# Performance work log

Hardware: AMD Instinct MI355X
Metric: run time of the kernel (lower is better)

Reference implementation:

```python
import jax, jax.numpy as jnp
import numpy as np

N_TX, N_USER, N_MERCH = 100000, 20000, 5000
E = 400000
F_IN, H, L = 32, 256, 2


def setup_inputs() -> dict:
    key = jax.random.key(0)
    ks = jax.random.split(key, 24)
    p = lambda k, s: 0.02 * jax.random.normal(k, s, dtype=jnp.float32)
    return {
        "x_tx": jax.random.normal(ks[0], (N_TX, F_IN), dtype=jnp.float32),
        "x_user": jax.random.normal(ks[1], (N_USER, H), dtype=jnp.float32),
        "x_merch": jax.random.normal(ks[2], (N_MERCH, H), dtype=jnp.float32),
        # input projection
        "Wp": p(ks[3], (F_IN, H)), "bp": jnp.zeros((H,), jnp.float32),
        # per-layer, per-edge-type SAGEConv params: lin_l (neighbor, with bias) and lin_r (root, no bias)
        "Wl": p(ks[4], (L, 4, H, H)), "bl": jnp.zeros((L, 4, H), jnp.float32),
        "Wr": p(ks[5], (L, 4, H, H)),
        # classifier head
        "Wc1": p(ks[6], (H, H // 2)), "bc1": jnp.zeros((H // 2,), jnp.float32),
        "Wc2": p(ks[7], (H // 2, 1)), "bc2": jnp.zeros((1,), jnp.float32),
        # revenue head
        "Wv1": p(ks[8], (H, H // 2)), "bv1": jnp.zeros((H // 2,), jnp.float32),
        "Wv2": p(ks[9], (H // 2, 1)), "bv2": jnp.zeros((1,), jnp.float32),
        # edge lists (src, dst) per relation
        "e_ut_src": jax.random.randint(ks[10], (E,), 0, N_USER, dtype=jnp.int32),
        "e_ut_dst": jax.random.randint(ks[11], (E,), 0, N_TX, dtype=jnp.int32),
        "e_tm_src": jax.random.randint(ks[12], (E,), 0, N_TX, dtype=jnp.int32),
        "e_tm_dst": jax.random.randint(ks[13], (E,), 0, N_MERCH, dtype=jnp.int32),
        "e_mt_src": jax.random.randint(ks[14], (E,), 0, N_MERCH, dtype=jnp.int32),
        "e_mt_dst": jax.random.randint(ks[15], (E,), 0, N_TX, dtype=jnp.int32),
        "e_tu_src": jax.random.randint(ks[16], (E,), 0, N_TX, dtype=jnp.int32),
        "e_tu_dst": jax.random.randint(ks[17], (E,), 0, N_USER, dtype=jnp.int32),
    }


def _seg_mean(x_src, src, dst, n_dst):
    # gather source features per edge, scatter-mean into destinations
    msg = x_src[src]                                        # [E, H]
    s = jax.ops.segment_sum(msg, dst, num_segments=n_dst)   # [n_dst, H]
    cnt = jax.ops.segment_sum(jnp.ones((dst.shape[0],), x_src.dtype), dst, num_segments=n_dst)
    return s / jnp.maximum(cnt, 1.0)[:, None]


def _sage(x_src, x_dst, src, dst, Wl, bl, Wr):
    # PyG SAGEConv: lin_l(mean_neighbors) + lin_r(x_dst)
    m = _seg_mean(x_src, src, dst, x_dst.shape[0])
    return m @ Wl + bl + x_dst @ Wr


def reference(x_tx, x_user, x_merch, Wp, bp, Wl, bl, Wr,
              Wc1, bc1, Wc2, bc2, Wv1, bv1, Wv2, bv2,
              e_ut_src, e_ut_dst, e_tm_src, e_tm_dst,
              e_mt_src, e_mt_dst, e_tu_src, e_tu_dst):
    xt = x_tx @ Wp + bp          # input_proj on 'transaction'
    xu, xm = x_user, x_merch     # already hidden_dim -> used as-is
    for l in range(L):
        t_from_u = _sage(xu, xt, e_ut_src, e_ut_dst, Wl[l, 0], bl[l, 0], Wr[l, 0])
        m_from_t = _sage(xt, xm, e_tm_src, e_tm_dst, Wl[l, 1], bl[l, 1], Wr[l, 1])
        t_from_m = _sage(xm, xt, e_mt_src, e_mt_dst, Wl[l, 2], bl[l, 2], Wr[l, 2])
        u_from_t = _sage(xt, xu, e_tu_src, e_tu_dst, Wl[l, 3], bl[l, 3], Wr[l, 3])
        # HeteroConv aggr='mean' over edge types per destination, then ReLU (dropout = identity in eval)
        xt = jax.nn.relu(0.5 * (t_from_u + t_from_m))
        xm = jax.nn.relu(m_from_t)
        xu = jax.nn.relu(u_from_t)
    fraud_logits = (jax.nn.relu(xt @ Wc1 + bc1) @ Wc2 + bc2)[:, 0]
    revenue_pred = (jax.nn.relu(xt @ Wv1 + bv1) @ Wv2 + bv2)[:, 0]
    return fraud_logits, revenue_pred
```

## Files before the change

### kernel.cpp

```cpp
#include <hip/hip_runtime.h>

#define NTX 100000
#define NUSER 20000
#define NMERCH 5000
#define HD 256
#define ROWPAD 128

using u16 = unsigned short;
typedef __attribute__((ext_vector_type(8))) short bf16x8;
typedef __attribute__((ext_vector_type(4))) float f32x4;

__device__ __forceinline__ u16 f2bf(float f){
  unsigned u = __float_as_uint(f);
  unsigned r = (u + 0x7FFFu + ((u >> 16) & 1u)) >> 16;
  return (u16)r;
}
__device__ __forceinline__ float bf2f(u16 b){
  return __uint_as_float(((unsigned)b) << 16);
}
__device__ __forceinline__ unsigned pk2(float a, float b){
  return (unsigned)f2bf(a) | ((unsigned)f2bf(b) << 16);
}

__device__ __forceinline__ void gather4(const u16* __restrict__ T, const int* __restrict__ ss,
    int j0, int j1, int lane, int c, float& o0, float& o1, float& o2, float& o3){
  float a0=0,a1=0,a2=0,a3=0, b0=0,b1=0,b2=0,b3=0;
  float c0=0,c1=0,c2=0,c3=0, d0=0,d1=0,d2=0,d3=0;
  for (int base = j0; base < j1; base += 64){
    int n = j1 - base; if (n > 64) n = 64;
    int idx = ss[base + (lane < n ? lane : 0)];
    for (int jj = 0; jj < n; jj += 4){
      int s0 = __shfl(idx, jj);
      int s1 = __shfl(idx, jj+1);
      int s2 = __shfl(idx, jj+2);
      int s3 = __shfl(idx, jj+3);
      ushort4 v0 = *(const ushort4*)(T + (size_t)s0*HD + c);
      ushort4 v1 = *(const ushort4*)(T + (size_t)s1*HD + c);
      ushort4 v2 = *(const ushort4*)(T + (size_t)s2*HD + c);
      ushort4 v3 = *(const ushort4*)(T + (size_t)s3*HD + c);
      a0 += bf2f(v0.x); a1 += bf2f(v0.y); a2 += bf2f(v0.z); a3 += bf2f(v0.w);
      if (jj+1 < n){ b0 += bf2f(v1.x); b1 += bf2f(v1.y); b2 += bf2f(v1.z); b3 += bf2f(v1.w); }
      if (jj+2 < n){ c0 += bf2f(v2.x); c1 += bf2f(v2.y); c2 += bf2f(v2.z); c3 += bf2f(v2.w); }
      if (jj+3 < n){ d0 += bf2f(v3.x); d1 += bf2f(v3.y); d2 += bf2f(v3.z); d3 += bf2f(v3.w); }
    }
  }
  o0 += (a0+b0)+(c0+d0); o1 += (a1+b1)+(c1+d1);
  o2 += (a2+b2)+(c2+d2); o3 += (a3+b3)+(c3+d3);
}

__device__ __forceinline__ int rel_n(int y){ return y==0?NTX: y==1?NMERCH: y==2?NTX:NUSER; }
__device__ __forceinline__ int rel_coff(int y){ return y==0?0: y==1?100000: y==2?105000:205000; }
__device__ __forceinline__ int rel_rpoff(int y){ return y==0?0: y==1?100001: y==2?105002:205003; }
__device__ __forceinline__ int rel_shift(int y){ return y==0?11: y==1?8: y==2?11:10; }
__device__ __forceinline__ int rel_np(int y){ return y==0?49: y==1?20: y==2?49:20; }
#define ECH 128
#define PSTW 72

__global__ __launch_bounds__(256) void csrA_kernel(const int* __restrict__ d0p, const int* __restrict__ d1p,
    const int* __restrict__ d2p, const int* __restrict__ d3p, int nE, int* __restrict__ PC){
  int y = blockIdx.y;
  const int* dst = y==0?d0p: y==1?d1p: y==2?d2p:d3p;
  int shift = rel_shift(y);
  __shared__ int cc[64];
  int t = threadIdx.x;
  if (t < 64) cc[t] = 0;
  __syncthreads();
  int CH = (nE + ECH - 1)/ECH;
  int e0 = blockIdx.x*CH, e1 = e0 + CH; if (e1 > nE) e1 = nE;
  for (int e = e0 + t*4; e < e1; e += 1024){
    int a = dst[e];
    int b = (e+1 < e1) ? dst[e+1] : -1;
    int c = (e+2 < e1) ? dst[e+2] : -1;
    int d = (e+3 < e1) ? dst[e+3] : -1;
    atomicAdd(&cc[a>>shift], 1);
    if (b >= 0) atomicAdd(&cc[b>>shift], 1);
    if (c >= 0) atomicAdd(&cc[c>>shift], 1);
    if (d >= 0) atomicAdd(&cc[d>>shift], 1);
  }
  __syncthreads();
  if (t < 64) PC[(((size_t)y*ECH + blockIdx.x)<<6) + t] = cc[t];
}

__global__ void csrB_kernel(int* __restrict__ PC, int* __restrict__ PST, int* __restrict__ RP, int nE){
  int y = blockIdx.y;
  int np = rel_np(y);
  int t = threadIdx.x;
  __shared__ int sh[64];
  int run = 0;
  if (t < np){
    for (int c = 0; c < ECH; ++c){
      size_t idx = (((size_t)y*ECH + c)<<6) + t;
      int v = PC[idx]; PC[idx] = run; run += v;
    }
  }
  sh[t] = run;
  __syncthreads();
  if (t == 0){
    int acc = 0;
    for (int i = 0; i < np; ++i){ int v = sh[i]; sh[i] = acc; acc += v; }
    PST[y*PSTW + np] = nE;
    RP[rel_rpoff(y) + rel_n(y)] = nE;
  }
  __syncthreads();
  if (t < np){
    int base = sh[t];
    PST[y*PSTW + t] = base;
    for (int c = 0; c < ECH; ++c){
      size_t idx = (((size_t)y*ECH + c)<<6) + t;
      PC[idx] += base;
    }
  }
}

__global__ __launch_bounds__(256) void csrC_kernel(
    const int* __restrict__ s0p, const int* __restrict__ d0p,
    const int* __restrict__ s1p, const int* __restrict__ d1p,
    const int* __restrict__ s2p, const int* __restrict__ d2p,
    const int* __restrict__ s3p, const int* __restrict__ d3p,
    const int* __restrict__ PC, int* __restrict__ EB, int nE){
  int y = blockIdx.y;
  const int* src = y==0?s0p: y==1?s1p: y==2?s2p:s3p;
  const int* dst = y==0?d0p: y==1?d1p: y==2?d2p:d3p;
  int shift = rel_shift(y);
  int mask = (1<<shift) - 1;
  __shared__ int cur[64];
  int t = threadIdx.x;
  if (t < 64) cur[t] = PC[(((size_t)y*ECH + blockIdx.x)<<6) + t];
  __syncthreads();
  int CH = (nE + ECH - 1)/ECH;
  int e0 = blockIdx.x*CH, e1 = e0 + CH; if (e1 > nE) e1 = nE;
  int* eb = EB + (size_t)y*nE;
  for (int e = e0 + t*4; e < e1; e += 1024){
    #pragma unroll
    for (int u = 0; u < 4; ++u){
      int ee = e + u;
      if (ee < e1){
        int d = dst[ee], s = src[ee];
        int pos = atomicAdd(&cur[d>>shift], 1);
        eb[pos] = ((d & mask) << 17) | s;
      }
    }
  }
}

__global__ __launch_bounds__(256) void csrD_kernel(const int* __restrict__ EB, const int* __restrict__ PST,
    int* __restrict__ RP, float* __restrict__ INV,
    int* __restrict__ ss0, int* __restrict__ ss1, int* __restrict__ ss2, int* __restrict__ ss3, int nE){
  int y = blockIdx.y;
  int np = rel_np(y);
  int part = blockIdx.x;
  if (part >= np) return;
  int shift = rel_shift(y);
  int n = rel_n(y);
  int gbase = part << shift;
  int len = n - gbase; int range = 1 << shift; if (len > range) len = range;
  __shared__ int cnt[2048];
  __shared__ int curs[2048];
  __shared__ int sh[256];
  int t = threadIdx.x;
  for (int i = t; i < len; i += 256) cnt[i] = 0;
  __syncthreads();
  const int* eb = EB + (size_t)y*nE;
  int j0 = PST[y*PSTW + part], j1 = PST[y*PSTW + part + 1];
  for (int j = j0 + t*4; j < j1; j += 1024){
    int a = eb[j];
    int b = (j+1 < j1) ? eb[j+1] : -1;
    int c = (j+2 < j1) ? eb[j+2] : -1;
    int d = (j+3 < j1) ? eb[j+3] : -1;
    atomicAdd(&cnt[a>>17], 1);
    if (b >= 0) atomicAdd(&cnt[b>>17], 1);
    if (c >= 0) atomicAdd(&cnt[c>>17], 1);
    if (d >= 0) atomicAdd(&cnt[d>>17], 1);
  }
  __syncthreads();
  int base8 = t*8;
  int vals[8]; int tsum = 0;
  #pragma unroll
  for (int u = 0; u < 8; ++u){
    int i = base8 + u;
    int v = (i < len) ? cnt[i] : 0;
    vals[u] = tsum; tsum += v;
  }
  sh[t] = tsum;
  __syncthreads();
  for (int o = 1; o < 256; o <<= 1){
    int v = (t >= o) ? sh[t-o] : 0;
    __syncthreads();
    sh[t] += v;
    __syncthreads();
  }
  int tbase = j0 + sh[t] - tsum;
  int rpo = rel_rpoff(y) + gbase;
  int ivo = rel_coff(y) + gbase;
  #pragma unroll
  for (int u = 0; u < 8; ++u){
    int i = base8 + u;
    if (i < len){
      int start = tbase + vals[u];
      curs[i] = start;
      RP[rpo + i] = start;
      INV[ivo + i] = 1.f/fmaxf((float)cnt[i], 1.f);
    }
  }
  __syncthreads();
  int* ss = y==0?ss0: y==1?ss1: y==2?ss2:ss3;
  for (int j = j0 + t*4; j < j1; j += 1024){
    #pragma unroll
    for (int u = 0; u < 4; ++u){
      int jj = j + u;
      if (jj < j1){
        int pk = eb[jj];
        int pos = atomicAdd(&curs[pk>>17], 1);
        ss[pos] = pk & 0x1FFFF;
      }
    }
  }
}

__global__ __launch_bounds__(256) void wprep_kernel(const float* __restrict__ Wl, const float* __restrict__ Wr,
    const float* __restrict__ Wp, const float* __restrict__ Wc1, const float* __restrict__ Wv1,
    const float* __restrict__ bc1, const float* __restrict__ bv1,
    u16* __restrict__ WTl, u16* __restrict__ WTr1, u16* __restrict__ WTr3, u16* __restrict__ WT02,
    u16* __restrict__ WTH, u16* __restrict__ WTp, float* __restrict__ bH){
  int y = blockIdx.y;
  int i = blockIdx.x*256 + threadIdx.x;
  if (y < 8){
    if (i < 65536){ int k=i>>8, n=i&255; WTl[(size_t)y*65536 + n*256 + k] = f2bf(Wl[(size_t)y*65536 + i]); }
  } else if (y < 10){
    int l = y-8;
    if (i < 65536){ int k=i>>8, n=i&255; WTr1[(size_t)l*65536 + n*256 + k] = f2bf(Wr[(size_t)(l*4+1)*65536 + i]); }
  } else if (y < 12){
    int l = y-10;
    if (i < 65536){ int k=i>>8, n=i&255; WTr3[(size_t)l*65536 + n*256 + k] = f2bf(Wr[(size_t)(l*4+3)*65536 + i]); }
  } else if (y < 14){
    int l = y-12;
    if (i < 65536){ int k=i>>8, n=i&255;
      WT02[(size_t)l*65536 + n*256 + k] = f2bf(Wr[(size_t)(l*4+0)*65536 + i] + Wr[(size_t)(l*4+2)*65536 + i]); }
  } else if (y == 14){
    if (i < 65536){ int k=i>>8, n=i&255;
      float v = (n < 128) ? Wc1[k*128 + n] : Wv1[k*128 + (n-128)];
      WTH[(size_t)n*256 + k] = f2bf(v); }
  } else {
    if (i < 8192){ int k=i>>8, n=i&255; WTp[(size_t)n*32 + k] = f2bf(Wp[i]); }
    if (i < 256) bH[i] = (i < 128) ? bc1[i] : bv1[i-128];
  }
}

__global__ __launch_bounds__(256) void cvt2_kernel(const float* __restrict__ xu,
    const float* __restrict__ xm, u16* __restrict__ XU, u16* __restrict__ XM){
  int y = blockIdx.y;
  const float* in = y==0?xu:xm;
  u16* out = y==0?XU:XM;
  int n4 = y==0?NUSER*HD/4:NMERCH*HD/4;
  int i = blockIdx.x*256 + threadIdx.x;
  if (i >= n4) return;
  float4 v = ((const float4*)in)[i];
  ushort4 o; o.x = f2bf(v.x); o.y = f2bf(v.y); o.z = f2bf(v.z); o.w = f2bf(v.w);
  ((ushort4*)out)[i] = o;
}

#define STAGE_STORE(EXPR_BF16)                                                     \
  {                                                                                \
    int rsub = (lane >> 4) << 2;                                                   \
    int wh = w >> 1;                                                               \
    for (int h = 0; h < 2; ++h){                                                   \
      if (wh == h){                                                                \
        _Pragma("unroll")                                                          \
        for (int j = 0; j < 4; ++j){                                               \
          int cl = wn + j*16 + lm;                                                 \
          _Pragma("unroll")                                                        \
          for (int i = 0; i < 4; ++i){                                             \
            int lr = i*16 + rsub;                                                  \
            _Pragma("unroll")                                                      \
            for (int r = 0; r < 4; ++r) smem[(lr+r)*136 + cl] = (EXPR_BF16);       \
          }                                                                        \
        }                                                                          \
      }                                                                            \
      __syncthreads();                                                             \
      int lr2 = threadIdx.x >> 2;                                                  \
      int cb = (threadIdx.x & 3) << 5;                                             \
      int grow = m0 + h*64 + lr2;                                                  \
      if (grow < M){                                                               \
        _Pragma("unroll")                                                          \
        for (int kq = 0; kq < 4; ++kq)                                             \
          *(uint4*)(C + (size_t)grow*256 + n0 + cb + kq*8) =                       \
              *(const uint4*)&smem[lr2*136 + cb + kq*8];                           \
      }                                                                            \
      __syncthreads();                                                             \
    }                                                                              \
  }

__global__ __launch_bounds__(256) void proj_gemm_kernel(const float* __restrict__ A, const u16* __restrict__ WT,
    const float* __restrict__ bias, u16* __restrict__ C, int M){
  __shared__ u16 smem[10240];
  u16* As = smem; u16* Bs = smem + 5120;
  int m0 = blockIdx.x * 128, n0 = blockIdx.y * 128;
  int t = threadIdx.x;
  int w = t >> 6, lane = t & 63;
  int wm = (w >> 1) << 6, wn = (w & 1) << 6;
  int lm = lane & 15;
  int lk = (lane >> 4) << 3;
  int sr = t >> 1, sc = (t & 1) << 4;
  float4 f0 = {0,0,0,0}, f1 = {0,0,0,0}, f2 = {0,0,0,0}, f3 = {0,0,0,0};
  if (m0 + sr < M){
    const float* ap = A + (size_t)(m0+sr)*32 + sc;
    f0 = *(const float4*)(ap+0); f1 = *(const float4*)(ap+4);
    f2 = *(const float4*)(ap+8); f3 = *(const float4*)(ap+12);
  }
  uint4 q0, q1;
  q0.x = pk2(f0.x,f0.y); q0.y = pk2(f0.z,f0.w); q0.z = pk2(f1.x,f1.y); q0.w = pk2(f1.z,f1.w);
  q1.x = pk2(f2.x,f2.y); q1.y = pk2(f2.z,f2.w); q1.z = pk2(f3.x,f3.y); q1.w = pk2(f3.z,f3.w);
  *(uint4*)&As[sr*40 + sc] = q0;
  *(uint4*)&As[sr*40 + sc+8] = q1;
  const u16* bp_ = WT + (size_t)(n0+sr)*32 + sc;
  *(uint4*)&Bs[sr*40 + sc]   = *(const uint4*)(bp_);
  *(uint4*)&Bs[sr*40 + sc+8] = *(const uint4*)(bp_ + 8);
  __syncthreads();
  bf16x8 af[4], bf[4];
  #pragma unroll
  for (int i = 0; i < 4; ++i) af[i] = *(const bf16x8*)&As[(wm + i*16 + lm)*40 + lk];
  #pragma unroll
  for (int j = 0; j < 4; ++j) bf[j] = *(const bf16x8*)&Bs[(wn + j*16 + lm)*40 + lk];
  f32x4 acc[4][4] = {};
  #pragma unroll
  for (int i = 0; i < 4; ++i)
    #pragma unroll
    for (int j = 0; j < 4; ++j)
      acc[i][j] = __builtin_amdgcn_mfma_f32_16x16x32_bf16(af[i], bf[j], acc[i][j], 0, 0, 0);
  __syncthreads();
  float bcol[4];
  #pragma unroll
  for (int j = 0; j < 4; ++j) bcol[j] = bias[n0 + wn + j*16 + lm];
  STAGE_STORE(f2bf(acc[i][j][r] + bcol[j]))
}

__global__ __launch_bounds__(256) void gemm_nb_kernel(const u16* __restrict__ A, const u16* __restrict__ WT,
    u16* __restrict__ C, int M){
  __shared__ u16 smem[10240];
  u16* As = smem; u16* Bs = smem + 5120;
  int m0 = blockIdx.x * 128, n0 = blockIdx.y * 128;
  if (m0 >= M) return;
  int t = threadIdx.x;
  int w = t >> 6, lane = t & 63;
  int wm = (w >> 1) << 6, wn = (w & 1) << 6;
  int lm = lane & 15;
  int lk = (lane >> 4) << 3;
  f32x4 acc[4][4] = {};
  int sr0 = t >> 2, sk0 = (t & 3) << 3;
  int sr1 = sr0 + 64;
  for (int k0 = 0; k0 < 256; k0 += 32){
    uint4 a0 = *(const uint4*)(A  + (size_t)(m0+sr0)*256 + k0 + sk0);
    uint4 a1 = *(const uint4*)(A  + (size_t)(m0+sr1)*256 + k0 + sk0);
    uint4 b0 = *(const uint4*)(WT + (size_t)(n0+sr0)*256 + k0 + sk0);
    uint4 b1 = *(const uint4*)(WT + (size_t)(n0+sr1)*256 + k0 + sk0);
    *(uint4*)&As[sr0*40 + sk0] = a0;
    *(uint4*)&As[sr1*40 + sk0] = a1;
    *(uint4*)&Bs[sr0*40 + sk0] = b0;
    *(uint4*)&Bs[sr1*40 + sk0] = b1;
    __syncthreads();
    bf16x8 af[4], bf[4];
    #pragma unroll
    for (int i = 0; i < 4; ++i) af[i] = *(const bf16x8*)&As[(wm + i*16 + lm)*40 + lk];
    #pragma unroll
    for (int j = 0; j < 4; ++j) bf[j] = *(const bf16x8*)&Bs[(wn + j*16 + lm)*40 + lk];
    #pragma unroll
    for (int i = 0; i < 4; ++i)
      #pragma unroll
      for (int j = 0; j < 4; ++j)
        acc[i][j] = __builtin_amdgcn_mfma_f32_16x16x32_bf16(af[i], bf[j], acc[i][j], 0, 0, 0);
    __syncthreads();
  }
  STAGE_STORE(f2bf(acc[i][j][r]))
}

__global__ __launch_bounds__(256) void pair_gemm_kernel(
    const u16* __restrict__ A0, const u16* __restrict__ W0, u16* __restrict__ C0, int M0,
    const u16* __restrict__ A1, const u16* __restrict__ W1, u16* __restrict__ C1, int M1){
  int z = blockIdx.z;
  const u16* A = z ? A1 : A0;
  const u16* WT = z ? W1 : W0;
  u16* C = z ? C1 : C0;
  int M = z ? M1 : M0;
  int m0 = blockIdx.x * 128, n0 = blockIdx.y * 128;
  if (m0 >= M) return;
  __shared__ u16 smem[10240];
  u16* As = smem; u16* Bs = smem + 5120;
  int t = threadIdx.x;
  int w = t >> 6, lane = t & 63;
  int wm = (w >> 1) << 6, wn = (w & 1) << 6;
  int lm = lane & 15;
  int lk = (lane >> 4) << 3;
  f32x4 acc[4][4] = {};
  int sr0 = t >> 2, sk0 = (t & 3) << 3;
  int sr1 = sr0 + 64;
  for (int k0 = 0; k0 < 256; k0 += 32){
    uint4 a0 = *(const uint4*)(A  + (size_t)(m0+sr0)*256 + k0 + sk0);
    uint4 a1 = *(const uint4*)(A  + (size_t)(m0+sr1)*256 + k0 + sk0);
    uint4 b0 = *(const uint4*)(WT + (size_t)(n0+sr0)*256 + k0 + sk0);
    uint4 b1 = *(const uint4*)(WT + (size_t)(n0+sr1)*256 + k0 + sk0);
    *(uint4*)&As[sr0*40 + sk0] = a0;
    *(uint4*)&As[sr1*40 + sk0] = a1;
    *(uint4*)&Bs[sr0*40 + sk0] = b0;
    *(uint4*)&Bs[sr1*40 + sk0] = b1;
    __syncthreads();
    bf16x8 af[4], bf[4];
    #pragma unroll
    for (int i = 0; i < 4; ++i) af[i] = *(const bf16x8*)&As[(wm + i*16 + lm)*40 + lk];
    #pragma unroll
    for (int j = 0; j < 4; ++j) bf[j] = *(const bf16x8*)&Bs[(wn + j*16 + lm)*40 + lk];
    #pragma unroll
    for (int i = 0; i < 4; ++i)
      #pragma unroll
      for (int j = 0; j < 4; ++j)
        acc[i][j] = __builtin_amdgcn_mfma_f32_16x16x32_bf16(af[i], bf[j], acc[i][j], 0, 0, 0);
    __syncthreads();
  }
  STAGE_STORE(f2bf(acc[i][j][r]))
}

__global__ __launch_bounds__(256) void pair_gemm2_kernel(
    const u16* __restrict__ G0, const u16* __restrict__ X0, const u16* __restrict__ Wa0, const u16* __restrict__ Wb0,
    const float* __restrict__ b0, u16* __restrict__ C0, int M0,
    const u16* __restrict__ G1, const u16* __restrict__ X1, const u16* __restrict__ Wa1, const u16* __restrict__ Wb1,
    const float* __restrict__ b1, u16* __restrict__ C1, int M1){
  int z = blockIdx.z;
  const u16* G  = z ? G1 : G0;
  const u16* X  = z ? X1 : X0;
  const u16* Wa = z ? Wa1 : Wa0;
  const u16* Wb = z ? Wb1 : Wb0;
  const float* bias = z ? b1 : b0;
  u16* C = z ? C1 : C0;
  int M = z ? M1 : M0;
  int m0 = blockIdx.x * 128, n0 = blockIdx.y * 128;
  if (m0 >= M) return;
  __shared__ u16 smem[10240];
  u16* As = smem; u16* Bs = smem + 5120;
  int t = threadIdx.x;
  int w = t >> 6, lane = t & 63;
  int wm = (w >> 1) << 6, wn = (w & 1) << 6;
  int lm = lane & 15;
  int lk = (lane >> 4) << 3;
  f32x4 acc[4][4] = {};
  int sr0 = t >> 2, sk0 = (t & 3) << 3;
  int sr1 = sr0 + 64;
  for (int k0 = 0; k0 < 512; k0 += 32){
    const u16* A  = (k0 < 256) ? G : X;
    const u16* WT = (k0 < 256) ? Wa : Wb;
    int kk = k0 & 255;
    uint4 a0 = *(const uint4*)(A  + (size_t)(m0+sr0)*256 + kk + sk0);
    uint4 a1 = *(const uint4*)(A  + (size_t)(m0+sr1)*256 + kk + sk0);
    uint4 b0_ = *(const uint4*)(WT + (size_t)(n0+sr0)*256 + kk + sk0);
    uint4 b1_ = *(const uint4*)(WT + (size_t)(n0+sr1)*256 + kk + sk0);
    *(uint4*)&As[sr0*40 + sk0] = a0;
    *(uint4*)&As[sr1*40 + sk0] = a1;
    *(uint4*)&Bs[sr0*40 + sk0] = b0_;
    *(uint4*)&Bs[sr1*40 + sk0] = b1_;
    __syncthreads();
    bf16x8 af[4], bf[4];
    #pragma unroll
    for (int i = 0; i < 4; ++i) af[i] = *(const bf16x8*)&As[(wm + i*16 + lm)*40 + lk];
    #pragma unroll
    for (int j = 0; j < 4; ++j) bf[j] = *(const bf16x8*)&Bs[(wn + j*16 + lm)*40 + lk];
    #pragma unroll
    for (int i = 0; i < 4; ++i)
      #pragma unroll
      for (int j = 0; j < 4; ++j)
        acc[i][j] = __builtin_amdgcn_mfma_f32_16x16x32_bf16(af[i], bf[j], acc[i][j], 0, 0, 0);
    __syncthreads();
  }
  float bcol[4];
  #pragma unroll
  for (int j = 0; j < 4; ++j) bcol[j] = bias[n0 + wn + j*16 + lm];
  STAGE_STORE(f2bf(fmaxf(acc[i][j][r] + bcol[j], 0.f)))
}

__global__ __launch_bounds__(256) void gather_pair_kernel(const u16* __restrict__ XT,
    const int* __restrict__ rp0, const int* __restrict__ ss0, const float* __restrict__ inv0,
    u16* __restrict__ out0, int M0,
    const int* __restrict__ rp1, const int* __restrict__ ss1, const float* __restrict__ inv1,
    u16* __restrict__ out1, int M1){
  int y = blockIdx.y;
  const int* rp = y ? rp1 : rp0;
  const int* ss = y ? ss1 : ss0;
  const float* inv = y ? inv1 : inv0;
  u16* out = y ? out1 : out0;
  int M = y ? M1 : M0;
  int d = blockIdx.x*4 + (threadIdx.x >> 6);
  if (d >= M) return;
  int lane = threadIdx.x & 63;
  int c = lane << 2;
  float o0=0,o1=0,o2=0,o3=0;
  gather4(XT, ss, rp[d], rp[d+1], lane, c, o0, o1, o2, o3);
  float sc = inv[d];
  ushort4 o; o.x = f2bf(o0*sc); o.y = f2bf(o1*sc); o.z = f2bf(o2*sc); o.w = f2bf(o3*sc);
  *(ushort4*)(out + (size_t)d*HD + c) = o;
}

__global__ __launch_bounds__(256) void fused_tx_kernel(const u16* __restrict__ ACCb,
    const u16* __restrict__ Tu, const u16* __restrict__ Tm,
    const int* __restrict__ rpu, const int* __restrict__ ssu, const float* __restrict__ invu,
    const int* __restrict__ rpm, const int* __restrict__ ssm, const float* __restrict__ invm,
    const float* __restrict__ b0, const float* __restrict__ b2, u16* __restrict__ XT, int M){
  int d = blockIdx.x*4 + (threadIdx.x >> 6);
  if (d >= M) return;
  int lane = threadIdx.x & 63;
  int c = lane << 2;
  ushort4 av = *(const ushort4*)(ACCb + (size_t)d*HD + c);
  float r0 = bf2f(av.x), r1 = bf2f(av.y), r2 = bf2f(av.z), r3 = bf2f(av.w);
  {
    float s0=0,s1=0,s2=0,s3=0;
    gather4(Tu, ssu, rpu[d], rpu[d+1], lane, c, s0, s1, s2, s3);
    float sc = invu[d];
    r0 += s0*sc; r1 += s1*sc; r2 += s2*sc; r3 += s3*sc;
  }
  {
    float s0=0,s1=0,s2=0,s3=0;
    gather4(Tm, ssm, rpm[d], rpm[d+1], lane, c, s0, s1, s2, s3);
    float sc = invm[d];
    r0 += s0*sc; r1 += s1*sc; r2 += s2*sc; r3 += s3*sc;
  }
  float4 bb0 = *(const float4*)(b0 + c);
  float4 bb2 = *(const float4*)(b2 + c);
  ushort4 o;
  o.x = f2bf(fmaxf(0.5f*(r0 + bb0.x + bb2.x), 0.f));
  o.y = f2bf(fmaxf(0.5f*(r1 + bb0.y + bb2.y), 0.f));
  o.z = f2bf(fmaxf(0.5f*(r2 + bb0.z + bb2.z), 0.f));
  o.w = f2bf(fmaxf(0.5f*(r3 + bb0.w + bb2.w), 0.f));
  *(ushort4*)(XT + (size_t)d*HD + c) = o;
}

__global__ __launch_bounds__(256) void fused_head_kernel(const u16* __restrict__ A, const u16* __restrict__ BT,
    const float* __restrict__ bias, const float* __restrict__ Wc2, const float* __restrict__ bc2,
    const float* __restrict__ Wv2, const float* __restrict__ bv2, float* __restrict__ out, int M){
  __shared__ u16 As[128*40];
  __shared__ u16 Bs[128*40];
  __shared__ float hpart[128];
  int m0 = blockIdx.x * 128, n0 = blockIdx.y * 128;
  int t = threadIdx.x;
  int w = t >> 6, lane = t & 63;
  int wm = (w >> 1) << 6, wn = (w & 1) << 6;
  int lm = lane & 15;
  int lk = (lane >> 4) << 3;
  if (t < 128) hpart[t] = 0.f;
  f32x4 acc[4][4] = {};
  int sr0 = t >> 2, sk0 = (t & 3) << 3;
  int sr1 = sr0 + 64;
  for (int k0 = 0; k0 < 256; k0 += 32){
    uint4 a0 = *(const uint4*)(A  + (size_t)(m0+sr0)*256 + k0 + sk0);
    uint4 a1 = *(const uint4*)(A  + (size_t)(m0+sr1)*256 + k0 + sk0);
    uint4 b0 = *(const uint4*)(BT + (size_t)(n0+sr0)*256 + k0 + sk0);
    uint4 b1 = *(const uint4*)(BT + (size_t)(n0+sr1)*256 + k0 + sk0);
    *(uint4*)&As[sr0*40 + sk0] = a0;
    *(uint4*)&As[sr1*40 + sk0] = a1;
    *(uint4*)&Bs[sr0*40 + sk0] = b0;
    *(uint4*)&Bs[sr1*40 + sk0] = b1;
    __syncthreads();
    bf16x8 af[4], bf[4];
    #pragma unroll
    for (int i = 0; i < 4; ++i) af[i] = *(const bf16x8*)&As[(wm + i*16 + lm)*40 + lk];
    #pragma unroll
    for (int j = 0; j < 4; ++j) bf[j] = *(const bf16x8*)&Bs[(wn + j*16 + lm)*40 + lk];
    #pragma unroll
    for (int i = 0; i < 4; ++i)
      #pragma unroll
      for (int j = 0; j < 4; ++j)
        acc[i][j] = __builtin_amdgcn_mfma_f32_16x16x32_bf16(af[i], bf[j], acc[i][j], 0, 0, 0);
    __syncthreads();
  }
  const float* w2 = blockIdx.y ? Wv2 : Wc2;
  float badd = blockIdx.y ? bv2[0] : bc2[0];
  size_t outoff = blockIdx.y ? (size_t)M : 0;
  int rsub = (lane >> 4) << 2;
  float w2v[4], bv[4];
  #pragma unroll
  for (int j = 0; j < 4; ++j){
    w2v[j] = w2[wn + j*16 + lm];
    bv[j]  = bias[n0 + wn + j*16 + lm];
  }
  #pragma unroll
  for (int i = 0; i < 4; ++i){
    #pragma unroll
    for (int r = 0; r < 4; ++r){
      float p = 0.f;
      #pragma unroll
      for (int j = 0; j < 4; ++j) p += fmaxf(acc[i][j][r] + bv[j], 0.f) * w2v[j];
      p += __shfl_xor(p, 1); p += __shfl_xor(p, 2);
      p += __shfl_xor(p, 4); p += __shfl_xor(p, 8);
      if (lm == 0) atomicAdd(&hpart[wm + i*16 + rsub + r], p);
    }
  }
  __syncthreads();
  if (t < 128){
    int row = m0 + t;
    if (row < M) out[outoff + row] = hpart[t] + badd;
  }
}

extern "C" void kernel_launch(void* const* d_in, const int* in_sizes, int n_in,
                              void* d_out, int out_size, void* d_ws, size_t ws_size,
                              hipStream_t stream){
  const float* x_tx   = (const float*)d_in[0];
  const float* x_user = (const float*)d_in[1];
  const float* x_merch= (const float*)d_in[2];
  const float* Wp  = (const float*)d_in[3];
  const float* bp  = (const float*)d_in[4];
  const float* Wl  = (const float*)d_in[5];
  const float* bl  = (const float*)d_in[6];
  const float* Wr  = (const float*)d_in[7];
  const float* Wc1 = (const float*)d_in[8];
  const float* bc1 = (const float*)d_in[9];
  const float* Wc2 = (const float*)d_in[10];
  const float* bc2 = (const float*)d_in[11];
  const float* Wv1 = (const float*)d_in[12];
  const float* bv1 = (const float*)d_in[13];
  const float* Wv2 = (const float*)d_in[14];
  const float* bv2 = (const float*)d_in[15];
  const int* e_ut_s = (const int*)d_in[16];
  const int* e_ut_d = (const int*)d_in[17];
  const int* e_tm_s = (const int*)d_in[18];
  const int* e_tm_d = (const int*)d_in[19];
  const int* e_mt_s = (const int*)d_in[20];
  const int* e_mt_d = (const int*)d_in[21];
  const int* e_tu_s = (const int*)d_in[22];
  const int* e_tu_d = (const int*)d_in[23];
  float* out = (float*)d_out;
  const int NE = in_sizes[16];

  char* p = (char*)d_ws;
  auto take = [&](size_t bytes)->char*{ char* r = p; p += (bytes + 255) & ~(size_t)255; return r; };
  u16*   XT    = (u16*)  take((size_t)(NTX+ROWPAD)*HD*2);
  u16*   ACCb  = (u16*)  take((size_t)(NTX+ROWPAD)*HD*2);
  u16*   Tu    = (u16*)  take((size_t)NUSER*HD*2);
  u16*   Tm    = (u16*)  take((size_t)NMERCH*HD*2);
  u16*   AGGU  = (u16*)  take((size_t)(NUSER+ROWPAD)*HD*2);
  u16*   AGGM  = (u16*)  take((size_t)(NMERCH+ROWPAD)*HD*2);
  u16*   XU0   = (u16*)  take((size_t)(NUSER+ROWPAD)*HD*2);
  u16*   XU1   = (u16*)  take((size_t)(NUSER+ROWPAD)*HD*2);
  u16*   XM0   = (u16*)  take((size_t)(NMERCH+ROWPAD)*HD*2);
  u16*   XM1   = (u16*)  take((size_t)(NMERCH+ROWPAD)*HD*2);
  float* INV   = (float*)take((size_t)225000*4);
  int*   RP    = (int*)  take((size_t)225008*4);
  int*   SS_ut = (int*)  take((size_t)NE*4);
  int*   SS_tm = (int*)  take((size_t)NE*4);
  int*   SS_mt = (int*)  take((size_t)NE*4);
  int*   SS_tu = (int*)  take((size_t)NE*4);
  int*   PC    = (int*)  take((size_t)4*ECH*64*4);
  int*   PST   = (int*)  take((size_t)4*PSTW*4);
  int*   EB    = (int*)  take((size_t)4*NE*4);
  u16*   WTp   = (u16*)  take((size_t)32*256*2);
  u16*   WTl   = (u16*)  take((size_t)8*65536*2);
  u16*   WTr1  = (u16*)  take((size_t)2*65536*2);
  u16*   WTr3  = (u16*)  take((size_t)2*65536*2);
  u16*   WT02  = (u16*)  take((size_t)2*65536*2);
  u16*   WTH   = (u16*)  take((size_t)65536*2);
  float* bH    = (float*)take((size_t)256*4);

  float* inv_ut = INV,  *inv_tm = INV+100000, *inv_mt = INV+105000, *inv_tu = INV+205000;
  int*   rp_ut  = RP,   *rp_tm  = RP+100001,  *rp_mt  = RP+105002,  *rp_tu  = RP+205003;

  csrA_kernel<<<dim3(ECH,4),256,0,stream>>>(e_ut_d, e_tm_d, e_mt_d, e_tu_d, NE, PC);
  csrB_kernel<<<dim3(1,4),64,0,stream>>>(PC, PST, RP, NE);
  csrC_kernel<<<dim3(ECH,4),256,0,stream>>>(e_ut_s, e_ut_d, e_tm_s, e_tm_d, e_mt_s, e_mt_d,
      e_tu_s, e_tu_d, PC, EB, NE);
  csrD_kernel<<<dim3(49,4),256,0,stream>>>(EB, PST, RP, INV, SS_ut, SS_tm, SS_mt, SS_tu, NE);

  wprep_kernel<<<dim3(256,16),256,0,stream>>>(Wl, Wr, Wp, Wc1, Wv1, bc1, bv1,
      WTl, WTr1, WTr3, WT02, WTH, WTp, bH);

  cvt2_kernel<<<dim3(5000,2),256,0,stream>>>(x_user, x_merch, XU0, XM0);
  proj_gemm_kernel<<<dim3(782,2),256,0,stream>>>(x_tx, WTp, bp, XT, NTX);

  u16* xu_cur = XU0; u16* xu_nxt = XU1;
  u16* xm_cur = XM0; u16* xm_nxt = XM1;

  for (int l = 0; l < 2; ++l){
    const float* bl_l = bl + (size_t)l*4*256;
    u16* WTl_l = WTl + (size_t)l*4*65536;

    gather_pair_kernel<<<dim3(5000,2),256,0,stream>>>(XT,
        rp_tm, SS_tm, inv_tm, AGGM, NMERCH,
        rp_tu, SS_tu, inv_tu, AGGU, NUSER);

    pair_gemm_kernel<<<dim3(157,2,2),256,0,stream>>>(
        xu_cur, WTl_l + 0*65536, Tu, NUSER,
        xm_cur, WTl_l + 2*65536, Tm, NMERCH);

    gemm_nb_kernel<<<dim3(782,2),256,0,stream>>>(XT, WT02 + (size_t)l*65536, ACCb, NTX);
    fused_tx_kernel<<<(NTX+3)/4,256,0,stream>>>(ACCb, Tu, Tm,
        rp_ut, SS_ut, inv_ut, rp_mt, SS_mt, inv_mt,
        bl_l + 0*256, bl_l + 2*256, XT, NTX);

    pair_gemm2_kernel<<<dim3(157,2,2),256,0,stream>>>(
        AGGU, xu_cur, WTl_l + 3*65536, WTr3 + (size_t)l*65536, bl_l + 3*256, xu_nxt, NUSER,
        AGGM, xm_cur, WTl_l + 1*65536, WTr1 + (size_t)l*65536, bl_l + 1*256, xm_nxt, NMERCH);

    { u16* tmp = xu_cur; xu_cur = xu_nxt; xu_nxt = tmp; }
    { u16* tmp = xm_cur; xm_cur = xm_nxt; xm_nxt = tmp; }
  }

  fused_head_kernel<<<dim3(782,2),256,0,stream>>>(XT, WTH, bH, Wc2, bc2, Wv2, bv2, out, NTX);
}
```

Measured before the change: 542.2 us.

## Merge per-layer GEMMs and gathers into two grouped launches with ping-pong XT

Each layer's three neighbor/root GEMMs (XT·WT02, xu·Wl0, xm·Wl2) now run in one flat-grid launch. The two gathers into merchant/user plus the fused transaction update run in a second flat-grid launch. The transaction state is double-buffered so the fused update writes in place into the ACC buffer and the gathers keep reading the old XT, which removes the ordering that forced separate launches. This cuts launches per layer from four to two and lets small workloads share the GPU with large ones, at the cost of branchy block dispatch and mixed block types inside one grid.

```diff
diff --git a/kernel.cpp b/kernel.cpp
--- a/kernel.cpp
+++ b/kernel.cpp
@@ -334,12 +334,9 @@
   STAGE_STORE(f2bf(acc[i][j][r] + bcol[j]))
 }
 
-__global__ __launch_bounds__(256) void gemm_nb_kernel(const u16* __restrict__ A, const u16* __restrict__ WT,
-    u16* __restrict__ C, int M){
-  __shared__ u16 smem[10240];
+__device__ __forceinline__ void gemm_nb_body(const u16* __restrict__ A, const u16* __restrict__ WT,
+    u16* __restrict__ C, int M, int m0, int n0, u16* smem){
   u16* As = smem; u16* Bs = smem + 5120;
-  int m0 = blockIdx.x * 128, n0 = blockIdx.y * 128;
-  if (m0 >= M) return;
   int t = threadIdx.x;
   int w = t >> 6, lane = t & 63;
   int wm = (w >> 1) << 6, wn = (w & 1) << 6;
@@ -373,49 +370,91 @@
   STAGE_STORE(f2bf(acc[i][j][r]))
 }
 
-__global__ __launch_bounds__(256) void pair_gemm_kernel(
-    const u16* __restrict__ A0, const u16* __restrict__ W0, u16* __restrict__ C0, int M0,
-    const u16* __restrict__ A1, const u16* __restrict__ W1, u16* __restrict__ C1, int M1){
-  int z = blockIdx.z;
-  const u16* A = z ? A1 : A0;
-  const u16* WT = z ? W1 : W0;
-  u16* C = z ? C1 : C0;
-  int M = z ? M1 : M0;
-  int m0 = blockIdx.x * 128, n0 = blockIdx.y * 128;
-  if (m0 >= M) return;
+__global__ __launch_bounds__(256) void gemmsA_kernel(
+    const u16* __restrict__ XT, const u16* __restrict__ WT02l, u16* __restrict__ ACCb,
+    const u16* __restrict__ xu, const u16* __restrict__ Wl0, u16* __restrict__ Tu,
+    const u16* __restrict__ xm, const u16* __restrict__ Wl2, u16* __restrict__ Tm){
   __shared__ u16 smem[10240];
-  u16* As = smem; u16* Bs = smem + 5120;
-  int t = threadIdx.x;
-  int w = t >> 6, lane = t & 63;
-  int wm = (w >> 1) << 6, wn = (w & 1) << 6;
-  int lm = lane & 15;
-  int lk = (lane >> 4) << 3;
-  f32x4 acc[4][4] = {};
-  int sr0 = t >> 2, sk0 = (t & 3) << 3;
-  int sr1 = sr0 + 64;
-  for (int k0 = 0; k0 < 256; k0 += 32){
-    uint4 a0 = *(const uint4*)(A  + (size_t)(m0+sr0)*256 + k0 + sk0);
-    uint4 a1 = *(const uint4*)(A  + (size_t)(m0+sr1)*256 + k0 + sk0);
-    uint4 b0 = *(const uint4*)(WT + (size_t)(n0+sr0)*256 + k0 + sk0);
-    uint4 b1 = *(const uint4*)(WT + (size_t)(n0+sr1)*256 + k0 + sk0);
-    *(uint4*)&As[sr0*40 + sk0] = a0;
-    *(uint4*)&As[sr1*40 + sk0] = a1;
-    *(uint4*)&Bs[sr0*40 + sk0] = b0;
-    *(uint4*)&Bs[sr1*40 + sk0] = b1;
-    __syncthreads();
-    bf16x8 af[4], bf[4];
-    #pragma unroll
-    for (int i = 0; i < 4; ++i) af[i] = *(const bf16x8*)&As[(wm + i*16 + lm)*40 + lk];
-    #pragma unroll
-    for (int j = 0; j < 4; ++j) bf[j] = *(const bf16x8*)&Bs[(wn + j*16 + lm)*40 + lk];
-    #pragma unroll
-    for (int i = 0; i < 4; ++i)
-      #pragma unroll
-      for (int j = 0; j < 4; ++j)
-        acc[i][j] = __builtin_amdgcn_mfma_f32_16x16x32_bf16(af[i], bf[j], acc[i][j], 0, 0, 0);
-    __syncthreads();
-  }
-  STAGE_STORE(f2bf(acc[i][j][r]))
+  int b = blockIdx.x;
+  if (b < 1564){
+    int ny = (b >= 782) ? 1 : 0;
+    int x = b - ny*782;
+    gemm_nb_body(XT, WT02l, ACCb, NTX, x*128, ny*128, smem);
+  } else {
+    int bb = b - 1564;
+    if (bb < 314){
+      int ny = bb / 157, x = bb - ny*157;
+      gemm_nb_body(xu, Wl0, Tu, NUSER, x*128, ny*128, smem);
+    } else {
+      bb -= 314;
+      int ny = bb / 40, x = bb - ny*40;
+      gemm_nb_body(xm, Wl2, Tm, NMERCH, x*128, ny*128, smem);
+    }
+  }
+}
+
+__device__ __forceinline__ void gather_body(const u16* __restrict__ XT,
+    const int* __restrict__ rp, const int* __restrict__ ss, const float* __restrict__ inv,
+    u16* __restrict__ out, int M, int bx){
+  int d = bx*4 + (threadIdx.x >> 6);
+  if (d >= M) return;
+  int lane = threadIdx.x & 63;
+  int c = lane << 2;
+  float o0=0,o1=0,o2=0,o3=0;
+  gather4(XT, ss, rp[d], rp[d+1], lane, c, o0, o1, o2, o3);
+  float sc = inv[d];
+  ushort4 o; o.x = f2bf(o0*sc); o.y = f2bf(o1*sc); o.z = f2bf(o2*sc); o.w = f2bf(o3*sc);
+  *(ushort4*)(out + (size_t)d*HD + c) = o;
+}
+
+__device__ __forceinline__ void fused_tx_body(const u16* __restrict__ ACCb,
+    const u16* __restrict__ Tu, const u16* __restrict__ Tm,
+    const int* __restrict__ rpu, const int* __restrict__ ssu, const float* __restrict__ invu,
+    const int* __restrict__ rpm, const int* __restrict__ ssm, const float* __restrict__ invm,
+    const float* __restrict__ b0, const float* __restrict__ b2, u16* __restrict__ XT, int M, int bx){
+  int d = bx*4 + (threadIdx.x >> 6);
+  if (d >= M) return;
+  int lane = threadIdx.x & 63;
+  int c = lane << 2;
+  ushort4 av = *(const ushort4*)(ACCb + (size_t)d*HD + c);
+  float r0 = bf2f(av.x), r1 = bf2f(av.y), r2 = bf2f(av.z), r3 = bf2f(av.w);
+  {
+    float s0=0,s1=0,s2=0,s3=0;
+    gather4(Tu, ssu, rpu[d], rpu[d+1], lane, c, s0, s1, s2, s3);
+    float sc = invu[d];
+    r0 += s0*sc; r1 += s1*sc; r2 += s2*sc; r3 += s3*sc;
+  }
+  {
+    float s0=0,s1=0,s2=0,s3=0;
+    gather4(Tm, ssm, rpm[d], rpm[d+1], lane, c, s0, s1, s2, s3);
+    float sc = invm[d];
+    r0 += s0*sc; r1 += s1*sc; r2 += s2*sc; r3 += s3*sc;
+  }
+  float4 bb0 = *(const float4*)(b0 + c);
+  float4 bb2 = *(const float4*)(b2 + c);
+  ushort4 o;
+  o.x = f2bf(fmaxf(0.5f*(r0 + bb0.x + bb2.x), 0.f));
+  o.y = f2bf(fmaxf(0.5f*(r1 + bb0.y + bb2.y), 0.f));
+  o.z = f2bf(fmaxf(0.5f*(r2 + bb0.z + bb2.z), 0.f));
+  o.w = f2bf(fmaxf(0.5f*(r3 + bb0.w + bb2.w), 0.f));
+  *(ushort4*)(XT + (size_t)d*HD + c) = o;
+}
+
+__global__ __launch_bounds__(256) void gatherB_kernel(const u16* __restrict__ XTc,
+    const int* __restrict__ rp_tm, const int* __restrict__ ss_tm, const float* __restrict__ inv_tm, u16* __restrict__ AGGM,
+    const int* __restrict__ rp_tu, const int* __restrict__ ss_tu, const float* __restrict__ inv_tu, u16* __restrict__ AGGU,
+    u16* __restrict__ ACCb, const u16* __restrict__ Tu, const u16* __restrict__ Tm,
+    const int* __restrict__ rp_ut, const int* __restrict__ ss_ut, const float* __restrict__ inv_ut,
+    const int* __restrict__ rp_mt, const int* __restrict__ ss_mt, const float* __restrict__ inv_mt,
+    const float* __restrict__ b0, const float* __restrict__ b2){
+  int b = blockIdx.x;
+  if (b < 1250){
+    gather_body(XTc, rp_tm, ss_tm, inv_tm, AGGM, NMERCH, b);
+  } else if (b < 6250){
+    gather_body(XTc, rp_tu, ss_tu, inv_tu, AGGU, NUSER, b - 1250);
+  } else {
+    fused_tx_body(ACCb, Tu, Tm, rp_ut, ss_ut, inv_ut, rp_mt, ss_mt, inv_mt, b0, b2, ACCb, NTX, b - 6250);
+  }
 }
 
 __global__ __launch_bounds__(256) void pair_gemm2_kernel(
@@ -472,61 +511,6 @@
   #pragma unroll
   for (int j = 0; j < 4; ++j) bcol[j] = bias[n0 + wn + j*16 + lm];
   STAGE_STORE(f2bf(fmaxf(acc[i][j][r] + bcol[j], 0.f)))
-}
-
-__global__ __launch_bounds__(256) void gather_pair_kernel(const u16* __restrict__ XT,
-    const int* __restrict__ rp0, const int* __restrict__ ss0, const float* __restrict__ inv0,
-    u16* __restrict__ out0, int M0,
-    const int* __restrict__ rp1, const int* __restrict__ ss1, const float* __restrict__ inv1,
-    u16* __restrict__ out1, int M1){
-  int y = blockIdx.y;
-  const int* rp = y ? rp1 : rp0;
-  const int* ss = y ? ss1 : ss0;
-  const float* inv = y ? inv1 : inv0;
-  u16* out = y ? out1 : out0;
-  int M = y ? M1 : M0;
-  int d = blockIdx.x*4 + (threadIdx.x >> 6);
-  if (d >= M) return;
-  int lane = threadIdx.x & 63;
-  int c = lane << 2;
-  float o0=0,o1=0,o2=0,o3=0;
-  gather4(XT, ss, rp[d], rp[d+1], lane, c, o0, o1, o2, o3);
-  float sc = inv[d];
-  ushort4 o; o.x = f2bf(o0*sc); o.y = f2bf(o1*sc); o.z = f2bf(o2*sc); o.w = f2bf(o3*sc);
-  *(ushort4*)(out + (size_t)d*HD + c) = o;
-}
-
-__global__ __launch_bounds__(256) void fused_tx_kernel(const u16* __restrict__ ACCb,
-    const u16* __restrict__ Tu, const u16* __restrict__ Tm,
-    const int* __restrict__ rpu, const int* __restrict__ ssu, const float* __restrict__ invu,
-    const int* __restrict__ rpm, const int* __restrict__ ssm, const float* __restrict__ invm,
-    const float* __restrict__ b0, const float* __restrict__ b2, u16* __restrict__ XT, int M){
-  int d = blockIdx.x*4 + (threadIdx.x >> 6);
-  if (d >= M) return;
-  int lane = threadIdx.x & 63;
-  int c = lane << 2;
-  ushort4 av = *(const ushort4*)(ACCb + (size_t)d*HD + c);
-  float r0 = bf2f(av.x), r1 = bf2f(av.y), r2 = bf2f(av.z), r3 = bf2f(av.w);
-  {
-    float s0=0,s1=0,s2=0,s3=0;
-    gather4(Tu, ssu, rpu[d], rpu[d+1], lane, c, s0, s1, s2, s3);
-    float sc = invu[d];
-    r0 += s0*sc; r1 += s1*sc; r2 += s2*sc; r3 += s3*sc;
-  }
-  {
-    float s0=0,s1=0,s2=0,s3=0;
-    gather4(Tm, ssm, rpm[d], rpm[d+1], lane, c, s0, s1, s2, s3);
-    float sc = invm[d];
-    r0 += s0*sc; r1 += s1*sc; r2 += s2*sc; r3 += s3*sc;
-  }
-  float4 bb0 = *(const float4*)(b0 + c);
-  float4 bb2 = *(const float4*)(b2 + c);
-  ushort4 o;
-  o.x = f2bf(fmaxf(0.5f*(r0 + bb0.x + bb2.x), 0.f));
-  o.y = f2bf(fmaxf(0.5f*(r1 + bb0.y + bb2.y), 0.f));
-  o.z = f2bf(fmaxf(0.5f*(r2 + bb0.z + bb2.z), 0.f));
-  o.w = f2bf(fmaxf(0.5f*(r3 + bb0.w + bb2.w), 0.f));
-  *(ushort4*)(XT + (size_t)d*HD + c) = o;
 }
 
 __global__ __launch_bounds__(256) void fused_head_kernel(const u16* __restrict__ A, const u16* __restrict__ BT,
@@ -670,6 +654,7 @@
   cvt2_kernel<<<dim3(5000,2),256,0,stream>>>(x_user, x_merch, XU0, XM0);
   proj_gemm_kernel<<<dim3(782,2),256,0,stream>>>(x_tx, WTp, bp, XT, NTX);
 
+  u16* xt_cur  = XT;   u16* acc_buf = ACCb;
   u16* xu_cur = XU0; u16* xu_nxt = XU1;
   u16* xm_cur = XM0; u16* xm_nxt = XM1;
 
@@ -677,18 +662,18 @@
     const float* bl_l = bl + (size_t)l*4*256;
     u16* WTl_l = WTl + (size_t)l*4*65536;
 
-    gather_pair_kernel<<<dim3(5000,2),256,0,stream>>>(XT,
-        rp_tm, SS_tm, inv_tm, AGGM, NMERCH,
-        rp_tu, SS_tu, inv_tu, AGGU, NUSER);
-
-    pair_gemm_kernel<<<dim3(157,2,2),256,0,stream>>>(
-        xu_cur, WTl_l + 0*65536, Tu, NUSER,
-        xm_cur, WTl_l + 2*65536, Tm, NMERCH);
-
-    gemm_nb_kernel<<<dim3(782,2),256,0,stream>>>(XT, WT02 + (size_t)l*65536, ACCb, NTX);
-    fused_tx_kernel<<<(NTX+3)/4,256,0,stream>>>(ACCb, Tu, Tm,
+    gemmsA_kernel<<<1958,256,0,stream>>>(
+        xt_cur, WT02 + (size_t)l*65536, acc_buf,
+        xu_cur, WTl_l + 0*65536, Tu,
+        xm_cur, WTl_l + 2*65536, Tm);
+
+    gatherB_kernel<<<31250,256,0,stream>>>(xt_cur,
+        rp_tm, SS_tm, inv_tm, AGGM,
+        rp_tu, SS_tu, inv_tu, AGGU,
+        acc_buf, Tu, Tm,
         rp_ut, SS_ut, inv_ut, rp_mt, SS_mt, inv_mt,
-        bl_l + 0*256, bl_l + 2*256, XT, NTX);
+        bl_l + 0*256, bl_l + 2*256);
+    { u16* tmp = xt_cur; xt_cur = acc_buf; acc_buf = tmp; }
 
     pair_gemm2_kernel<<<dim3(157,2,2),256,0,stream>>>(
         AGGU, xu_cur, WTl_l + 3*65536, WTr3 + (size_t)l*65536, bl_l + 3*256, xu_nxt, NUSER,
@@ -698,5 +683,5 @@
     { u16* tmp = xm_cur; xm_cur = xm_nxt; xm_nxt = tmp; }
   }
 
-  fused_head_kernel<<<dim3(782,2),256,0,stream>>>(XT, WTH, bH, Wc2, bc2, Wv2, bv2, out, NTX);
-}
+  fused_head_kernel<<<dim3(782,2),256,0,stream>>>(xt_cur, WTH, bH, Wc2, bc2, Wv2, bv2, out, NTX);
+}
```

New measurement: 512.7 us, median of 2. 1.06x faster.
